# Optimization experiments

Measured on AMD Instinct MI355X. Metric: run time of the kernel, lower is better.

The kernel has to match this reference:

```python
import jax, jax.numpy as jnp
import numpy as np

B, S, D, H, F = 2, 2048, 1024, 16, 4096
HD = D // H
NEG_INF = jnp.float32(-1e30)


def layer_norm(x, gamma, beta, eps=1e-6):
    mu = jnp.mean(x, axis=-1, keepdims=True)
    var = jnp.mean(jnp.square(x - mu), axis=-1, keepdims=True)
    return (x - mu) * jax.lax.rsqrt(var + eps) * gamma + beta


def setup_inputs() -> dict:
    key = jax.random.key(0)
    ks = jax.random.split(key, 8)
    d = np.sqrt(float(D))
    dx_up = np.sqrt(6.0 / (D + F))
    dx_dn = np.sqrt(6.0 / (F + D))
    return {
        "x_embeds": jax.random.normal(ks[0], (B, S, D), dtype=jnp.float32),
        "tokens": jax.random.randint(ks[1], (B, S), 0, 128, dtype=jnp.int32),
        "KQV": jax.random.uniform(ks[2], (D, 3 * D), jnp.float32, -1 / d, 1 / d),
        "WO": jax.random.uniform(ks[3], (D, D), jnp.float32, -1 / d, 1 / d),
        "W_up": jax.random.uniform(ks[4], (D, F), jnp.float32, -dx_up, dx_up),
        "b_up": jnp.zeros((F,), jnp.float32),
        "W_down": jax.random.uniform(ks[5], (F, D), jnp.float32, -dx_dn, dx_dn),
        "b_down": jnp.zeros((D,), jnp.float32),
        "ln1_g": jnp.ones((D,), jnp.float32),
        "ln1_b": jnp.zeros((D,), jnp.float32),
        "ln2_g": jnp.ones((D,), jnp.float32),
        "ln2_b": jnp.zeros((D,), jnp.float32),
        "start_token_id": 1,
    }


def reference(x_embeds, tokens, KQV, WO, W_up, b_up, W_down, b_down,
              ln1_g, ln1_b, ln2_g, ln2_b, start_token_id):
    b, s = x_embeds.shape[0], x_embeds.shape[1]
    # --- attention ---
    x_kqv = jnp.einsum("bsd,de->bse", x_embeds, KQV)          # [B,S,3D]
    x_kqv = x_kqv.reshape(b, s, H, 3, HD)
    k = x_kqv[:, :, :, 0, :]   # [B,S,H,HD]
    q = x_kqv[:, :, :, 1, :]
    v = x_kqv[:, :, :, 2, :]
    inner = jnp.einsum("bqhd,bkhd->bhqk", q, k)               # [B,H,S,S]
    # causal mask
    causal = jnp.tril(jnp.ones((s, s), dtype=bool))           # [S,S]
    # block-diagonal document mask from start tokens
    seg = jnp.cumsum((tokens == start_token_id).astype(jnp.int32), axis=1)  # [B,S]
    same_seg = seg[:, :, None] == seg[:, None, :]             # [B,S,S]
    mask = causal[None, None] & same_seg[:, None]             # [B,1->H,S,S]
    inner = jnp.where(mask, inner, NEG_INF)
    dk = jnp.sqrt(jnp.float32(HD))
    WA = jax.nn.softmax(inner / dk, axis=-1)
    head_outs = jnp.einsum("bhqk,bkhd->bqhd", WA, v)          # [B,S,H,HD]
    out = head_outs.reshape(b, s, D) @ WO
    out = layer_norm(out, ln1_g, ln1_b)
    x = out + x_embeds
    # --- ffnn ---
    h = jax.nn.relu(x @ W_up + b_up)
    out = h @ W_down + b_down
    out = layer_norm(out, ln2_g, ln2_b)
    return out + x
```

## Files before the change

kernel.cpp:

```cpp
#include <hip/hip_runtime.h>

typedef unsigned short u16;
typedef unsigned int u32;
typedef __bf16 bf16_t;
typedef bf16_t bf16x8 __attribute__((ext_vector_type(8)));
typedef u16 u16x8 __attribute__((ext_vector_type(8)));
typedef float f32x4 __attribute__((ext_vector_type(4)));

__device__ __forceinline__ float bf2f(u16 u) {
    union { float f; unsigned i; } c; c.i = ((unsigned)u) << 16; return c.f;
}
__device__ __forceinline__ u16 f2bf(float f) {
    return __builtin_bit_cast(u16, (bf16_t)f);
}
__device__ __forceinline__ f32x4 mfma16(bf16x8 a, bf16x8 b, f32x4 c) {
    return __builtin_amdgcn_mfma_f32_16x16x32_bf16(a, b, c, 0, 0, 0);
}
__device__ __forceinline__ void gld16(const u16* g, u16* l) {
    __builtin_amdgcn_global_load_lds(
        (const __attribute__((address_space(1))) void*)g,
        (__attribute__((address_space(3))) void*)l, 16, 0, 0);
}

__global__ __launch_bounds__(256)
void cvt_kernel(const float* __restrict__ in, u16* __restrict__ out)
{
    const int i = (blockIdx.x * 256 + threadIdx.x) * 8;
    float4 a = *reinterpret_cast<const float4*>(in + i);
    float4 b = *reinterpret_cast<const float4*>(in + i + 4);
    u16x8 o;
    o[0] = f2bf(a.x); o[1] = f2bf(a.y); o[2] = f2bf(a.z); o[3] = f2bf(a.w);
    o[4] = f2bf(b.x); o[5] = f2bf(b.y); o[6] = f2bf(b.z); o[7] = f2bf(b.w);
    *reinterpret_cast<u16x8*>(out + i) = o;
}

__global__ __launch_bounds__(256)
void cvt_t_kernel(const float* __restrict__ in, u16* __restrict__ out,
                  int K, int N)
{
    __shared__ float tile[32][33];
    const int kb = blockIdx.x * 32, nb = blockIdx.y * 32;
    const int r = threadIdx.x >> 3, c4 = threadIdx.x & 7;
    float4 v = *reinterpret_cast<const float4*>(&in[(size_t)(kb + r) * N + nb + c4 * 4]);
    tile[r][c4 * 4 + 0] = v.x; tile[r][c4 * 4 + 1] = v.y;
    tile[r][c4 * 4 + 2] = v.z; tile[r][c4 * 4 + 3] = v.w;
    __syncthreads();
    ushort4 o;
    o.x = f2bf(tile[c4 * 4 + 0][r]);
    o.y = f2bf(tile[c4 * 4 + 1][r]);
    o.z = f2bf(tile[c4 * 4 + 2][r]);
    o.w = f2bf(tile[c4 * 4 + 3][r]);
    *reinterpret_cast<ushort4*>(&out[(size_t)(nb + r) * K + kb + c4 * 4]) = o;
}

template<int BM, int NSPLIT, bool BIAS, bool RELU, bool QSCALE>
__global__ __launch_bounds__(256)
void gemm_kernel(const u16* __restrict__ A, const u16* __restrict__ Bt,
                 const float* __restrict__ bias, u16* __restrict__ C,
                 int M, int N, int K)
{
    __shared__ u16 As[2][BM][32];
    __shared__ u16 Bs[2][128][32];
    constexpr int AI = BM / 32;
    const int tid  = threadIdx.x;
    const int lane = tid & 63;
    const int wid  = tid >> 6;
    const int wm = wid >> 1, wn = wid & 1;
    const int bm = blockIdx.x, bn = blockIdx.y;
    const int kg = lane >> 4;
    const int lc = lane & 15;
    const int pk = kg ^ ((lc + (lc >> 2)) & 3);

    f32x4 acc[AI][4];
    #pragma unroll
    for (int i = 0; i < AI; ++i)
        #pragma unroll
        for (int j = 0; j < 4; ++j)
            acc[i][j] = f32x4{0.f, 0.f, 0.f, 0.f};

    const int nk = (K >> 5) / NSPLIT;
    const int kbase = (NSPLIT > 1) ? blockIdx.z * nk : 0;

    auto stage = [&](int kt, int b) {
        int ktg = kbase + kt;
        #pragma unroll
        for (int p = 0; p < BM / 64; ++p) {
            int c = wid * BM + p * 64 + lane;
            int ko = (((c & 3) ^ (((c >> 2) + (c >> 4)) & 3))) * 8;
            gld16(A + (size_t)(bm * BM + (c >> 2)) * K + ktg * 32 + ko,
                  &As[b][0][0] + c * 8);
        }
        #pragma unroll
        for (int p = 0; p < 2; ++p) {
            int c = wid * 128 + p * 64 + lane;
            int ko = (((c & 3) ^ (((c >> 2) + (c >> 4)) & 3))) * 8;
            gld16(Bt + (size_t)(bn * 128 + (c >> 2)) * K + ktg * 32 + ko,
                  &Bs[b][0][0] + c * 8);
        }
    };

    stage(0, 0);
    __syncthreads();
    for (int kt = 0; kt < nk; ++kt) {
        const int cur = kt & 1;
        if (kt + 1 < nk) stage(kt + 1, cur ^ 1);
        bf16x8 af[AI], bf[4];
        #pragma unroll
        for (int i = 0; i < AI; ++i)
            af[i] = *reinterpret_cast<const bf16x8*>(&As[cur][wm * (BM / 2) + i * 16 + lc][pk * 8]);
        #pragma unroll
        for (int j = 0; j < 4; ++j)
            bf[j] = *reinterpret_cast<const bf16x8*>(&Bs[cur][wn * 64 + j * 16 + lc][pk * 8]);
        #pragma unroll
        for (int j = 0; j < 4; ++j)
            #pragma unroll
            for (int i = 0; i < AI; ++i)
                acc[i][j] = mfma16(af[i], bf[j], acc[i][j]);
        __syncthreads();
    }

    u16* Cp = C + (size_t)((NSPLIT > 1) ? blockIdx.z : 0) * M * N;
    const bool addb = BIAS && (NSPLIT == 1 || blockIdx.z == 0);
    #pragma unroll
    for (int i = 0; i < AI; ++i) {
        #pragma unroll
        for (int j = 0; j < 4; ++j) {
            int col = bn * 128 + wn * 64 + j * 16 + lc;
            float bv = addb ? bias[col] : 0.f;
            float qs = 1.0f;
            if (QSCALE) {
                u32 cm = (u32)col % 192u;
                if (cm >= 64u && cm < 128u) qs = 0.1803368875f;
            }
            #pragma unroll
            for (int r = 0; r < 4; ++r) {
                int row = bm * BM + wm * (BM / 2) + i * 16 + kg * 4 + r;
                float v = acc[i][j][r] + bv;
                if (RELU) v = v > 0.f ? v : 0.f;
                if (QSCALE) v *= qs;
                Cp[(size_t)row * N + col] = f2bf(v);
            }
        }
    }
}

__global__ __launch_bounds__(256)
void qlo_kernel(const int* __restrict__ tokens, const int* __restrict__ start_id,
                int* __restrict__ qlo)
{
    constexpr int S = 2048;
    __shared__ int part[256];
    __shared__ int pref[256];
    const int b = blockIdx.x, tid = threadIdx.x;
    const int sid = start_id[0];
    const int base = b * S + tid * 8;
    int f[8]; int loc = -1;
    #pragma unroll
    for (int j = 0; j < 8; ++j) {
        f[j] = (tokens[base + j] == sid) ? 1 : 0;
        if (f[j]) loc = tid * 8 + j;
    }
    part[tid] = loc;
    __syncthreads();
    if (tid == 0) {
        int run = -1;
        for (int i = 0; i < 256; ++i) { pref[i] = run; run = max(run, part[i]); }
    }
    __syncthreads();
    int run = pref[tid];
    #pragma unroll
    for (int j = 0; j < 8; ++j) {
        if (f[j]) run = tid * 8 + j;
        qlo[base + j] = max(run, 0);
    }
}

#define MASKVAL -60000.0f
#define MINIT   -30000.0f
__global__ __launch_bounds__(256)
void attn_kernel(const u16* __restrict__ qkv, const int* __restrict__ qloA,
                 u16* __restrict__ attn_out)
{
    constexpr int S = 2048, DQ = 3072;
    __shared__ u16 Ks[64][72];
    __shared__ u16 Vt[64][72];
    __shared__ u16 Pt[4][16][72];
    __shared__ int wm4[4];

    const int tid = threadIdx.x;
    const int lane = tid & 63, w = tid >> 6;
    const int kg = lane >> 4, lc = lane & 15;
    const int qt = blockIdx.x, h = blockIdx.y, b = blockIdx.z;
    const size_t rowbase = (size_t)b * S;
    const int colK = h * 192, colQ = colK + 64, colV = colK + 128;
    const int qrow = qt * 64 + w * 16 + lc;

    bf16x8 qf0, qf1;
    {
        const u16* qp = &qkv[(rowbase + qrow) * DQ + colQ];
        qf0 = *reinterpret_cast<const bf16x8*>(qp + kg * 8);
        qf1 = *reinterpret_cast<const bf16x8*>(qp + 32 + kg * 8);
    }
    const int myqlo = qloA[rowbase + qrow];

    int vmin = myqlo;
    #pragma unroll
    for (int m = 1; m < 16; m <<= 1) vmin = min(vmin, __shfl_xor(vmin, m));
    if (lane == 0) wm4[w] = vmin;
    __syncthreads();
    const int kb0 = min(min(wm4[0], wm4[1]), min(wm4[2], wm4[3])) >> 6;

    float m_ = MINIT, l_ = 0.f;
    f32x4 o[4];
    #pragma unroll
    for (int d = 0; d < 4; ++d) o[d] = f32x4{0.f, 0.f, 0.f, 0.f};

    const int kr = tid >> 3, kc = tid & 7;
    const int rpv = tid >> 3, chv = tid & 7;
    uint4 gk0, gk1, gv0, gv1;

    auto issue = [&](int kb) {
        const size_t base = rowbase + (size_t)kb * 64;
        gk0 = *reinterpret_cast<const uint4*>(&qkv[(base + kr) * DQ + colK + kc * 8]);
        gk1 = *reinterpret_cast<const uint4*>(&qkv[(base + 32 + kr) * DQ + colK + kc * 8]);
        const u16* vp = &qkv[(base + rpv * 2) * DQ + colV + chv * 8];
        gv0 = *reinterpret_cast<const uint4*>(vp);
        gv1 = *reinterpret_cast<const uint4*>(vp + DQ);
    };
    auto write_lds = [&]() {
        *reinterpret_cast<uint4*>(&Ks[kr][kc * 8]) = gk0;
        *reinterpret_cast<uint4*>(&Ks[32 + kr][kc * 8]) = gk1;
        u16x8 va = __builtin_bit_cast(u16x8, gv0);
        u16x8 vb = __builtin_bit_cast(u16x8, gv1);
        const int kp = (rpv * 2) ^ (chv << 3);
        #pragma unroll
        for (int j = 0; j < 8; ++j)
            *reinterpret_cast<u32*>(&Vt[chv * 8 + j][kp]) =
                (u32)va[j] | ((u32)vb[j] << 16);
    };

    issue(kb0);
    for (int kb = kb0; kb <= qt; ++kb) {
        write_lds();
        __syncthreads();
        if (kb < qt) issue(kb + 1);

        f32x4 sT[4];
        #pragma unroll
        for (int ks = 0; ks < 4; ++ks) {
            bf16x8 kf0 = *reinterpret_cast<const bf16x8*>(&Ks[ks * 16 + lc][kg * 8]);
            bf16x8 kf1 = *reinterpret_cast<const bf16x8*>(&Ks[ks * 16 + lc][32 + kg * 8]);
            f32x4 s = f32x4{0.f, 0.f, 0.f, 0.f};
            s = mfma16(kf0, qf0, s);
            s = mfma16(kf1, qf1, s);
            sT[ks] = s;
        }
        const int lo = myqlo - kb * 64, hi = qrow - kb * 64;
        #pragma unroll
        for (int ks = 0; ks < 4; ++ks) {
            #pragma unroll
            for (int r = 0; r < 4; ++r) {
                int kk = ks * 16 + kg * 4 + r;
                bool ok = (kk >= lo) && (kk <= hi);
                sT[ks][r] = ok ? sT[ks][r] : MASKVAL;
            }
        }
        float tm = fmaxf(fmaxf(fmaxf(sT[0][0], sT[0][1]), fmaxf(sT[0][2], sT[0][3])),
                         fmaxf(fmaxf(sT[1][0], sT[1][1]), fmaxf(sT[1][2], sT[1][3])));
        tm = fmaxf(tm, fmaxf(fmaxf(fmaxf(sT[2][0], sT[2][1]), fmaxf(sT[2][2], sT[2][3])),
                             fmaxf(fmaxf(sT[3][0], sT[3][1]), fmaxf(sT[3][2], sT[3][3]))));
        tm = fmaxf(tm, __shfl_xor(tm, 16));
        tm = fmaxf(tm, __shfl_xor(tm, 32));
        float mn = fmaxf(m_, tm);
        float al = exp2f(m_ - mn);
        m_ = mn;
        float ps = 0.f;
        #pragma unroll
        for (int ks = 0; ks < 4; ++ks) {
            ushort4 pw;
            float p0 = exp2f(sT[ks][0] - m_); ps += p0; pw.x = f2bf(p0);
            float p1 = exp2f(sT[ks][1] - m_); ps += p1; pw.y = f2bf(p1);
            float p2 = exp2f(sT[ks][2] - m_); ps += p2; pw.z = f2bf(p2);
            float p3 = exp2f(sT[ks][3] - m_); ps += p3; pw.w = f2bf(p3);
            *reinterpret_cast<ushort4*>(&Pt[w][lc][ks * 16 + kg * 4]) = pw;
        }
        ps += __shfl_xor(ps, 16);
        ps += __shfl_xor(ps, 32);
        l_ = l_ * al + ps;
        float alr[4];
        #pragma unroll
        for (int r = 0; r < 4; ++r) alr[r] = __shfl(al, kg * 4 + r);
        #pragma unroll
        for (int d = 0; d < 4; ++d)
            #pragma unroll
            for (int r = 0; r < 4; ++r) o[d][r] *= alr[r];

        #pragma unroll
        for (int kf = 0; kf < 2; ++kf) {
            bf16x8 pf = *reinterpret_cast<const bf16x8*>(&Pt[w][lc][kf * 32 + kg * 8]);
            #pragma unroll
            for (int d = 0; d < 4; ++d) {
                int vrow = d * 16 + lc;
                int b3 = (kf * 4 + kg) ^ ((vrow >> 3) & 7);
                bf16x8 vf = *reinterpret_cast<const bf16x8*>(&Vt[vrow][b3 * 8]);
                o[d] = mfma16(pf, vf, o[d]);
            }
        }
        __syncthreads();
    }

    float lr[4];
    #pragma unroll
    for (int r = 0; r < 4; ++r) lr[r] = __shfl(l_, kg * 4 + r);
    #pragma unroll
    for (int d = 0; d < 4; ++d)
        #pragma unroll
        for (int r = 0; r < 4; ++r) {
            float v = o[d][r] / fmaxf(lr[r], 1e-20f);
            int qo = qt * 64 + w * 16 + kg * 4 + r;
            attn_out[(rowbase + qo) * 1024 + h * 64 + d * 16 + lc] = f2bf(v);
        }
}

template<int NSPL, bool WRITE_BF>
__global__ __launch_bounds__(256)
void ln_kernel(const u16* __restrict__ in, const float* __restrict__ gam,
               const float* __restrict__ bet, const float* res,
               float* out_f, u16* __restrict__ out_bf)
{
    const int row = blockIdx.x;
    const int tid = threadIdx.x;
    const int lane = tid & 63, w = tid >> 6;
    __shared__ float red1[4], red2[4];

    const size_t base = (size_t)row * 1024 + tid * 4;
    float x0 = 0.f, x1 = 0.f, x2 = 0.f, x3 = 0.f;
    #pragma unroll
    for (int sp = 0; sp < NSPL; ++sp) {
        ushort4 xv = *reinterpret_cast<const ushort4*>(in + (size_t)sp * 4194304 + base);
        x0 += bf2f(xv.x); x1 += bf2f(xv.y); x2 += bf2f(xv.z); x3 += bf2f(xv.w);
    }

    float s = x0 + x1 + x2 + x3;
    #pragma unroll
    for (int m = 1; m < 64; m <<= 1) s += __shfl_xor(s, m);
    if (lane == 0) red1[w] = s;
    __syncthreads();
    float mu = (red1[0] + red1[1] + red1[2] + red1[3]) * (1.0f / 1024.0f);

    float d0 = x0 - mu, d1 = x1 - mu, d2 = x2 - mu, d3 = x3 - mu;
    float q = d0 * d0 + d1 * d1 + d2 * d2 + d3 * d3;
    #pragma unroll
    for (int m = 1; m < 64; m <<= 1) q += __shfl_xor(q, m);
    if (lane == 0) red2[w] = q;
    __syncthreads();
    float var = (red2[0] + red2[1] + red2[2] + red2[3]) * (1.0f / 1024.0f);
    float rs = rsqrtf(var + 1e-6f);

    float dd[4] = {d0, d1, d2, d3};
    #pragma unroll
    for (int e = 0; e < 4; ++e) {
        int col = tid * 4 + e;
        size_t idx = (size_t)row * 1024 + col;
        float y = dd[e] * rs * gam[col] + bet[col];
        float ov = y + res[idx];
        out_f[idx] = ov;
        if constexpr (WRITE_BF) out_bf[idx] = f2bf(ov);
    }
}

extern "C" void kernel_launch(void* const* d_in, const int* in_sizes, int n_in,
                              void* d_out, int out_size, void* d_ws, size_t ws_size,
                              hipStream_t stream)
{
    const float* x_emb = (const float*)d_in[0];
    const int* tokens  = (const int*)d_in[1];
    const float* KQV   = (const float*)d_in[2];
    const float* WO    = (const float*)d_in[3];
    const float* W_up  = (const float*)d_in[4];
    const float* b_up  = (const float*)d_in[5];
    const float* W_dn  = (const float*)d_in[6];
    const float* b_dn  = (const float*)d_in[7];
    const float* g1    = (const float*)d_in[8];
    const float* be1   = (const float*)d_in[9];
    const float* g2    = (const float*)d_in[10];
    const float* be2   = (const float*)d_in[11];
    const int* start   = (const int*)d_in[12];

    const size_t MiB = 1048576;
    char* ws = (char*)d_ws;
    u16* XB     = (u16*)(ws + 0);
    u16* qkv    = (u16*)(ws + 8 * MiB);
    u16* attn_o = (u16*)(ws + 32 * MiB);
    u16* KBt    = (u16*)(ws + 40 * MiB);
    int* qloA   = (int*)(ws + 46 * MiB);
    u16* WOBt   = (u16*)(ws + 0);
    u16* cpart  = (u16*)(ws + 8 * MiB);
    u16* x_bf   = (u16*)(ws + 0);
    u16* WUBt   = (u16*)(ws + 40 * MiB);
    u16* hbuf   = (u16*)(ws + 8 * MiB);
    u16* WDBt   = (u16*)(ws + 0);
    u16* fpart  = (u16*)(ws + 40 * MiB);
    float* x_f  = (float*)d_out;
    float* outp = (float*)d_out;

    cvt_kernel<<<2048, 256, 0, stream>>>(x_emb, XB);
    cvt_t_kernel<<<dim3(32, 96), 256, 0, stream>>>(KQV, KBt, 1024, 3072);
    qlo_kernel<<<2, 256, 0, stream>>>(tokens, start, qloA);
    gemm_kernel<128, 1, false, false, true><<<dim3(32, 24), 256, 0, stream>>>(XB, KBt, nullptr, qkv, 4096, 3072, 1024);
    cvt_t_kernel<<<dim3(32, 32), 256, 0, stream>>>(WO, WOBt, 1024, 1024);
    attn_kernel<<<dim3(32, 16, 2), 256, 0, stream>>>(qkv, qloA, attn_o);
    cvt_t_kernel<<<dim3(32, 128), 256, 0, stream>>>(W_up, WUBt, 1024, 4096);
    gemm_kernel<128, 2, false, false, false><<<dim3(32, 8, 2), 256, 0, stream>>>(attn_o, WOBt, nullptr, cpart, 4096, 1024, 1024);
    ln_kernel<2, true><<<4096, 256, 0, stream>>>(cpart, g1, be1, x_emb, x_f, x_bf);
    gemm_kernel<128, 1, true, true, false><<<dim3(32, 32), 256, 0, stream>>>(x_bf, WUBt, b_up, hbuf, 4096, 4096, 1024);
    cvt_t_kernel<<<dim3(128, 32), 256, 0, stream>>>(W_dn, WDBt, 4096, 1024);
    if (ws_size >= 72 * MiB) {
        gemm_kernel<128, 4, true, false, false><<<dim3(32, 8, 4), 256, 0, stream>>>(hbuf, WDBt, b_dn, fpart, 4096, 1024, 4096);
        ln_kernel<4, false><<<4096, 256, 0, stream>>>(fpart, g2, be2, x_f, outp, nullptr);
    } else if (ws_size >= 56 * MiB) {
        gemm_kernel<128, 2, true, false, false><<<dim3(32, 8, 2), 256, 0, stream>>>(hbuf, WDBt, b_dn, fpart, 4096, 1024, 4096);
        ln_kernel<2, false><<<4096, 256, 0, stream>>>(fpart, g2, be2, x_f, outp, nullptr);
    } else {
        gemm_kernel<64, 1, true, false, false><<<dim3(64, 8), 256, 0, stream>>>(hbuf, WDBt, b_dn, fpart, 4096, 1024, 4096);
        ln_kernel<1, false><<<4096, 256, 0, stream>>>(fpart, g2, be2, x_f, outp, nullptr);
    }
}
```

Measured before the change: 243.1 us.

## Add 256x256-tile GEMM kernel with 8 waves for QKV, up and down projections

Adds a new GEMM kernel with 256x256 output tiles, 512 threads (8 waves, each owning 128x64), a swizzled LDS layout and double-buffered direct-to-LDS loads with explicit waitcnt and scheduling barriers. It replaces the 128-row GEMM for the QKV, FFN-up and FFN-down projections. The larger tile raises arithmetic intensity and cuts redundant global/LDS traffic per FLOP. In exchange it uses more registers, holds 64 KB of LDS per block and launches far fewer blocks (e.g. 192 or 256), which may underfill the 256 CUs.

```diff
diff --git a/kernel.cpp b/kernel.cpp
--- a/kernel.cpp
+++ b/kernel.cpp
@@ -21,6 +21,7 @@
         (const __attribute__((address_space(1))) void*)g,
         (__attribute__((address_space(3))) void*)l, 16, 0, 0);
 }
+#define SCHED_FENCE() __builtin_amdgcn_sched_barrier(0)
 
 __global__ __launch_bounds__(256)
 void cvt_kernel(const float* __restrict__ in, u16* __restrict__ out)
@@ -51,6 +52,113 @@
     o.z = f2bf(tile[c4 * 4 + 2][r]);
     o.w = f2bf(tile[c4 * 4 + 3][r]);
     *reinterpret_cast<ushort4*>(&out[(size_t)(nb + r) * K + kb + c4 * 4]) = o;
+}
+
+template<int NSPLIT, bool BIAS, bool RELU, bool QSCALE>
+__global__ __launch_bounds__(512, 2)
+void gemm256_kernel(const u16* __restrict__ A, const u16* __restrict__ Bt,
+                    const float* __restrict__ bias, u16* __restrict__ C,
+                    int M, int N, int K)
+{
+    __shared__ u16 As[2][256][32];
+    __shared__ u16 Bs[2][256][32];
+    const int tid  = threadIdx.x;
+    const int lane = tid & 63;
+    const int wid  = tid >> 6;
+    const int wm = wid >> 2, wn = wid & 3;
+    const int bm = blockIdx.x, bn = blockIdx.y;
+    const int kg = lane >> 4;
+    const int lc = lane & 15;
+    const int pk = kg ^ ((lc + (lc >> 2)) & 3);
+
+    f32x4 acc[8][4];
+    #pragma unroll
+    for (int i = 0; i < 8; ++i)
+        #pragma unroll
+        for (int j = 0; j < 4; ++j)
+            acc[i][j] = f32x4{0.f, 0.f, 0.f, 0.f};
+
+    const int nk = (K >> 5) / NSPLIT;
+    const int kbase = (NSPLIT > 1) ? blockIdx.z * nk : 0;
+
+    auto stage = [&](int kt, int b) {
+        const int ktg = kbase + kt;
+        #pragma unroll
+        for (int p = 0; p < 2; ++p) {
+            int c = p * 512 + tid;
+            int row = c >> 2;
+            int ko = ((c & 3) ^ ((row + (row >> 2)) & 3)) * 8;
+            gld16(A + (size_t)(bm * 256 + row) * K + ktg * 32 + ko,
+                  &As[b][0][0] + c * 8);
+        }
+        #pragma unroll
+        for (int p = 0; p < 2; ++p) {
+            int c = p * 512 + tid;
+            int row = c >> 2;
+            int ko = ((c & 3) ^ ((row + (row >> 2)) & 3)) * 8;
+            gld16(Bt + (size_t)(bn * 256 + row) * K + ktg * 32 + ko,
+                  &Bs[b][0][0] + c * 8);
+        }
+    };
+
+    stage(0, 0);
+    stage(1, 1);
+    asm volatile("s_waitcnt vmcnt(4)" ::: "memory");
+    SCHED_FENCE();
+    __builtin_amdgcn_s_barrier();
+    SCHED_FENCE();
+
+    for (int kt = 0; kt < nk; ++kt) {
+        const int cur = kt & 1;
+        bf16x8 af[8], bf[4];
+        #pragma unroll
+        for (int i = 0; i < 8; ++i)
+            af[i] = *reinterpret_cast<const bf16x8*>(&As[cur][wm * 128 + i * 16 + lc][pk * 8]);
+        #pragma unroll
+        for (int j = 0; j < 4; ++j)
+            bf[j] = *reinterpret_cast<const bf16x8*>(&Bs[cur][wn * 64 + j * 16 + lc][pk * 8]);
+        #pragma unroll
+        for (int j = 0; j < 4; ++j)
+            #pragma unroll
+            for (int i = 0; i < 8; ++i)
+                acc[i][j] = mfma16(af[i], bf[j], acc[i][j]);
+        SCHED_FENCE();
+        __builtin_amdgcn_s_barrier();
+        SCHED_FENCE();
+        if (kt + 2 < nk) {
+            stage(kt + 2, cur);
+            asm volatile("s_waitcnt vmcnt(4)" ::: "memory");
+        } else {
+            asm volatile("s_waitcnt vmcnt(0)" ::: "memory");
+        }
+        SCHED_FENCE();
+        __builtin_amdgcn_s_barrier();
+        SCHED_FENCE();
+    }
+
+    u16* Cp = C + (size_t)((NSPLIT > 1) ? blockIdx.z : 0) * M * N;
+    const bool addb = BIAS && (NSPLIT == 1 || blockIdx.z == 0);
+    #pragma unroll
+    for (int i = 0; i < 8; ++i) {
+        #pragma unroll
+        for (int j = 0; j < 4; ++j) {
+            int col = bn * 256 + wn * 64 + j * 16 + lc;
+            float bv = addb ? bias[col] : 0.f;
+            float qs = 1.0f;
+            if (QSCALE) {
+                u32 cm = (u32)col % 192u;
+                if (cm >= 64u && cm < 128u) qs = 0.1803368875f;
+            }
+            #pragma unroll
+            for (int r = 0; r < 4; ++r) {
+                int row = bm * 256 + wm * 128 + i * 16 + kg * 4 + r;
+                float v = acc[i][j][r] + bv;
+                if (RELU) v = v > 0.f ? v : 0.f;
+                if (QSCALE) v *= qs;
+                Cp[(size_t)row * N + col] = f2bf(v);
+            }
+        }
+    }
 }
 
 template<int BM, int NSPLIT, bool BIAS, bool RELU, bool QSCALE>
@@ -407,19 +515,19 @@
     cvt_kernel<<<2048, 256, 0, stream>>>(x_emb, XB);
     cvt_t_kernel<<<dim3(32, 96), 256, 0, stream>>>(KQV, KBt, 1024, 3072);
     qlo_kernel<<<2, 256, 0, stream>>>(tokens, start, qloA);
-    gemm_kernel<128, 1, false, false, true><<<dim3(32, 24), 256, 0, stream>>>(XB, KBt, nullptr, qkv, 4096, 3072, 1024);
+    gemm256_kernel<1, false, false, true><<<dim3(16, 12), 512, 0, stream>>>(XB, KBt, nullptr, qkv, 4096, 3072, 1024);
     cvt_t_kernel<<<dim3(32, 32), 256, 0, stream>>>(WO, WOBt, 1024, 1024);
     attn_kernel<<<dim3(32, 16, 2), 256, 0, stream>>>(qkv, qloA, attn_o);
     cvt_t_kernel<<<dim3(32, 128), 256, 0, stream>>>(W_up, WUBt, 1024, 4096);
     gemm_kernel<128, 2, false, false, false><<<dim3(32, 8, 2), 256, 0, stream>>>(attn_o, WOBt, nullptr, cpart, 4096, 1024, 1024);
     ln_kernel<2, true><<<4096, 256, 0, stream>>>(cpart, g1, be1, x_emb, x_f, x_bf);
-    gemm_kernel<128, 1, true, true, false><<<dim3(32, 32), 256, 0, stream>>>(x_bf, WUBt, b_up, hbuf, 4096, 4096, 1024);
+    gemm256_kernel<1, true, true, false><<<dim3(16, 16), 512, 0, stream>>>(x_bf, WUBt, b_up, hbuf, 4096, 4096, 1024);
     cvt_t_kernel<<<dim3(128, 32), 256, 0, stream>>>(W_dn, WDBt, 4096, 1024);
     if (ws_size >= 72 * MiB) {
-        gemm_kernel<128, 4, true, false, false><<<dim3(32, 8, 4), 256, 0, stream>>>(hbuf, WDBt, b_dn, fpart, 4096, 1024, 4096);
+        gemm256_kernel<4, true, false, false><<<dim3(16, 4, 4), 512, 0, stream>>>(hbuf, WDBt, b_dn, fpart, 4096, 1024, 4096);
         ln_kernel<4, false><<<4096, 256, 0, stream>>>(fpart, g2, be2, x_f, outp, nullptr);
     } else if (ws_size >= 56 * MiB) {
-        gemm_kernel<128, 2, true, false, false><<<dim3(32, 8, 2), 256, 0, stream>>>(hbuf, WDBt, b_dn, fpart, 4096, 1024, 4096);
+        gemm256_kernel<2, true, false, false><<<dim3(16, 4, 2), 512, 0, stream>>>(hbuf, WDBt, b_dn, fpart, 4096, 1024, 4096);
         ln_kernel<2, false><<<4096, 256, 0, stream>>>(fpart, g2, be2, x_f, outp, nullptr);
     } else {
         gemm_kernel<64, 1, true, false, false><<<dim3(64, 8), 256, 0, stream>>>(hbuf, WDBt, b_dn, fpart, 4096, 1024, 4096);
```

Result: slower. 248.1 us (+2.1%).

## Remap GEMM blocks per XCD for L2 locality and drop double buffering

Applied to the files above, without the earlier changes.

The GEMM now uses a 1D grid and remaps block ids so that the blocks landing on each XCD (id&7) cover a compact 16x(NBN/4) tile region, which should improve L2 reuse of A and B on the multi-die MI355X. It also replaces the double-buffered LDS pipeline with a single buffer that loads and then computes with two barriers per k-step, and fixes BM at 128, so the fallback path loses its BM=64 variant. The smaller LDS footprint may raise occupancy, but global loads no longer overlap with MFMA work within a block.

```diff
diff --git a/kernel.cpp b/kernel.cpp
--- a/kernel.cpp
+++ b/kernel.cpp
@@ -53,79 +53,79 @@
     *reinterpret_cast<ushort4*>(&out[(size_t)(nb + r) * K + kb + c4 * 4]) = o;
 }
 
-template<int BM, int NSPLIT, bool BIAS, bool RELU, bool QSCALE>
+template<int NBN, int NSPLIT, bool BIAS, bool RELU, bool QSCALE>
 __global__ __launch_bounds__(256)
 void gemm_kernel(const u16* __restrict__ A, const u16* __restrict__ Bt,
                  const float* __restrict__ bias, u16* __restrict__ C,
                  int M, int N, int K)
 {
-    __shared__ u16 As[2][BM][32];
-    __shared__ u16 Bs[2][128][32];
-    constexpr int AI = BM / 32;
+    __shared__ u16 As[128][32];
+    __shared__ u16 Bs[128][32];
     const int tid  = threadIdx.x;
     const int lane = tid & 63;
     const int wid  = tid >> 6;
     const int wm = wid >> 1, wn = wid & 1;
-    const int bm = blockIdx.x, bn = blockIdx.y;
+    constexpr int RBN = NBN / 4;
+    const int id  = blockIdx.x;
+    const int xcd = id & 7, j = id >> 3;
+    const int bm = (xcd & 1) * 16 + (j & 15);
+    const int bn = (xcd >> 1) * RBN + (j >> 4);
     const int kg = lane >> 4;
     const int lc = lane & 15;
     const int pk = kg ^ ((lc + (lc >> 2)) & 3);
 
-    f32x4 acc[AI][4];
-    #pragma unroll
-    for (int i = 0; i < AI; ++i)
-        #pragma unroll
-        for (int j = 0; j < 4; ++j)
-            acc[i][j] = f32x4{0.f, 0.f, 0.f, 0.f};
+    f32x4 acc[4][4];
+    #pragma unroll
+    for (int i = 0; i < 4; ++i)
+        #pragma unroll
+        for (int jj = 0; jj < 4; ++jj)
+            acc[i][jj] = f32x4{0.f, 0.f, 0.f, 0.f};
 
     const int nk = (K >> 5) / NSPLIT;
     const int kbase = (NSPLIT > 1) ? blockIdx.z * nk : 0;
 
-    auto stage = [&](int kt, int b) {
-        int ktg = kbase + kt;
-        #pragma unroll
-        for (int p = 0; p < BM / 64; ++p) {
-            int c = wid * BM + p * 64 + lane;
-            int ko = (((c & 3) ^ (((c >> 2) + (c >> 4)) & 3))) * 8;
-            gld16(A + (size_t)(bm * BM + (c >> 2)) * K + ktg * 32 + ko,
-                  &As[b][0][0] + c * 8);
-        }
+    for (int kt = 0; kt < nk; ++kt) {
+        const int ktg = kbase + kt;
+        __syncthreads();
         #pragma unroll
         for (int p = 0; p < 2; ++p) {
-            int c = wid * 128 + p * 64 + lane;
-            int ko = (((c & 3) ^ (((c >> 2) + (c >> 4)) & 3))) * 8;
-            gld16(Bt + (size_t)(bn * 128 + (c >> 2)) * K + ktg * 32 + ko,
-                  &Bs[b][0][0] + c * 8);
-        }
-    };
-
-    stage(0, 0);
-    __syncthreads();
-    for (int kt = 0; kt < nk; ++kt) {
-        const int cur = kt & 1;
-        if (kt + 1 < nk) stage(kt + 1, cur ^ 1);
-        bf16x8 af[AI], bf[4];
-        #pragma unroll
-        for (int i = 0; i < AI; ++i)
-            af[i] = *reinterpret_cast<const bf16x8*>(&As[cur][wm * (BM / 2) + i * 16 + lc][pk * 8]);
-        #pragma unroll
-        for (int j = 0; j < 4; ++j)
-            bf[j] = *reinterpret_cast<const bf16x8*>(&Bs[cur][wn * 64 + j * 16 + lc][pk * 8]);
-        #pragma unroll
-        for (int j = 0; j < 4; ++j)
+            int c = p * 256 + tid;
+            int row = c >> 2;
+            int ko = ((c & 3) ^ ((row + (row >> 2)) & 3)) * 8;
+            gld16(A + (size_t)(bm * 128 + row) * K + ktg * 32 + ko,
+                  &As[0][0] + c * 8);
+        }
+        #pragma unroll
+        for (int p = 0; p < 2; ++p) {
+            int c = p * 256 + tid;
+            int row = c >> 2;
+            int ko = ((c & 3) ^ ((row + (row >> 2)) & 3)) * 8;
+            gld16(Bt + (size_t)(bn * 128 + row) * K + ktg * 32 + ko,
+                  &Bs[0][0] + c * 8);
+        }
+        __syncthreads();
+
+        bf16x8 af[4], bf[4];
+        #pragma unroll
+        for (int i = 0; i < 4; ++i)
+            af[i] = *reinterpret_cast<const bf16x8*>(&As[wm * 64 + i * 16 + lc][pk * 8]);
+        #pragma unroll
+        for (int jj = 0; jj < 4; ++jj)
+            bf[jj] = *reinterpret_cast<const bf16x8*>(&Bs[wn * 64 + jj * 16 + lc][pk * 8]);
+        #pragma unroll
+        for (int jj = 0; jj < 4; ++jj)
             #pragma unroll
-            for (int i = 0; i < AI; ++i)
-                acc[i][j] = mfma16(af[i], bf[j], acc[i][j]);
-        __syncthreads();
+            for (int i = 0; i < 4; ++i)
+                acc[i][jj] = mfma16(af[i], bf[jj], acc[i][jj]);
     }
 
     u16* Cp = C + (size_t)((NSPLIT > 1) ? blockIdx.z : 0) * M * N;
     const bool addb = BIAS && (NSPLIT == 1 || blockIdx.z == 0);
     #pragma unroll
-    for (int i = 0; i < AI; ++i) {
-        #pragma unroll
-        for (int j = 0; j < 4; ++j) {
-            int col = bn * 128 + wn * 64 + j * 16 + lc;
+    for (int i = 0; i < 4; ++i) {
+        #pragma unroll
+        for (int jj = 0; jj < 4; ++jj) {
+            int col = bn * 128 + wn * 64 + jj * 16 + lc;
             float bv = addb ? bias[col] : 0.f;
             float qs = 1.0f;
             if (QSCALE) {
@@ -134,8 +134,8 @@
             }
             #pragma unroll
             for (int r = 0; r < 4; ++r) {
-                int row = bm * BM + wm * (BM / 2) + i * 16 + kg * 4 + r;
-                float v = acc[i][j][r] + bv;
+                int row = bm * 128 + wm * 64 + i * 16 + kg * 4 + r;
+                float v = acc[i][jj][r] + bv;
                 if (RELU) v = v > 0.f ? v : 0.f;
                 if (QSCALE) v *= qs;
                 Cp[(size_t)row * N + col] = f2bf(v);
@@ -407,22 +407,22 @@
     cvt_kernel<<<2048, 256, 0, stream>>>(x_emb, XB);
     cvt_t_kernel<<<dim3(32, 96), 256, 0, stream>>>(KQV, KBt, 1024, 3072);
     qlo_kernel<<<2, 256, 0, stream>>>(tokens, start, qloA);
-    gemm_kernel<128, 1, false, false, true><<<dim3(32, 24), 256, 0, stream>>>(XB, KBt, nullptr, qkv, 4096, 3072, 1024);
+    gemm_kernel<24, 1, false, false, true><<<768, 256, 0, stream>>>(XB, KBt, nullptr, qkv, 4096, 3072, 1024);
     cvt_t_kernel<<<dim3(32, 32), 256, 0, stream>>>(WO, WOBt, 1024, 1024);
     attn_kernel<<<dim3(32, 16, 2), 256, 0, stream>>>(qkv, qloA, attn_o);
     cvt_t_kernel<<<dim3(32, 128), 256, 0, stream>>>(W_up, WUBt, 1024, 4096);
-    gemm_kernel<128, 2, false, false, false><<<dim3(32, 8, 2), 256, 0, stream>>>(attn_o, WOBt, nullptr, cpart, 4096, 1024, 1024);
+    gemm_kernel<8, 2, false, false, false><<<dim3(256, 1, 2), 256, 0, stream>>>(attn_o, WOBt, nullptr, cpart, 4096, 1024, 1024);
     ln_kernel<2, true><<<4096, 256, 0, stream>>>(cpart, g1, be1, x_emb, x_f, x_bf);
-    gemm_kernel<128, 1, true, true, false><<<dim3(32, 32), 256, 0, stream>>>(x_bf, WUBt, b_up, hbuf, 4096, 4096, 1024);
+    gemm_kernel<32, 1, true, true, false><<<1024, 256, 0, stream>>>(x_bf, WUBt, b_up, hbuf, 4096, 4096, 1024);
     cvt_t_kernel<<<dim3(128, 32), 256, 0, stream>>>(W_dn, WDBt, 4096, 1024);
     if (ws_size >= 72 * MiB) {
-        gemm_kernel<128, 4, true, false, false><<<dim3(32, 8, 4), 256, 0, stream>>>(hbuf, WDBt, b_dn, fpart, 4096, 1024, 4096);
+        gemm_kernel<8, 4, true, false, false><<<dim3(256, 1, 4), 256, 0, stream>>>(hbuf, WDBt, b_dn, fpart, 4096, 1024, 4096);
         ln_kernel<4, false><<<4096, 256, 0, stream>>>(fpart, g2, be2, x_f, outp, nullptr);
     } else if (ws_size >= 56 * MiB) {
-        gemm_kernel<128, 2, true, false, false><<<dim3(32, 8, 2), 256, 0, stream>>>(hbuf, WDBt, b_dn, fpart, 4096, 1024, 4096);
+        gemm_kernel<8, 2, true, false, false><<<dim3(256, 1, 2), 256, 0, stream>>>(hbuf, WDBt, b_dn, fpart, 4096, 1024, 4096);
         ln_kernel<2, false><<<4096, 256, 0, stream>>>(fpart, g2, be2, x_f, outp, nullptr);
     } else {
-        gemm_kernel<64, 1, true, false, false><<<dim3(64, 8), 256, 0, stream>>>(hbuf, WDBt, b_dn, fpart, 4096, 1024, 4096);
+        gemm_kernel<8, 1, true, false, false><<<256, 256, 0, stream>>>(hbuf, WDBt, b_dn, fpart, 4096, 1024, 4096);
         ln_kernel<1, false><<<4096, 256, 0, stream>>>(fpart, g2, be2, x_f, outp, nullptr);
     }
 }
```

New measurement: 263.1 us. 1.08x slower.
